# Performance work log

Measured on AMD Instinct MI355X. Metric: run time of the kernel, lower is better.

Reference implementation:

```python
import jax, jax.numpy as jnp
import numpy as np

N_NODES = 100000
N_EDGES = 1600000
IN_CH = 128
HID = 128
N_REL = 8


def setup_inputs() -> dict:
    key = jax.random.key(0)
    k_x, k_src, k_dst, k_et, k_w, k_root, k_b = jax.random.split(key, 7)
    x = jax.random.normal(k_x, (N_NODES, IN_CH), dtype=jnp.float32)
    src = jax.random.randint(k_src, (N_EDGES,), 0, N_NODES)
    dst = jax.random.randint(k_dst, (N_EDGES,), 0, N_NODES)
    edge_index = jnp.stack([src, dst], axis=0)  # [2, E]
    edge_type = jax.random.randint(k_et, (N_EDGES,), 0, N_REL)
    # RGCNConv parameters: per-relation weight, root (self-loop) weight, bias
    scale = 1.0 / np.sqrt(IN_CH)
    W = jax.random.normal(k_w, (N_REL, IN_CH, HID), dtype=jnp.float32) * scale
    root = jax.random.normal(k_root, (IN_CH, HID), dtype=jnp.float32) * scale
    bias = jnp.zeros((HID,), dtype=jnp.float32)
    return {"x": x, "edge_index": edge_index, "edge_type": edge_type,
            "W": W, "root": root, "bias": bias}


def reference(x, edge_index, edge_type, W, root, bias):
    # RGCNConv (mean aggregation per relation) + ReLU. Dropout is identity (eval mode).
    # Aggregate-then-transform: mathematically identical to PyG's
    # transform-then-aggregate since the relation transform is linear,
    # but far cheaper (R matmuls over N nodes instead of E edges).
    N = x.shape[0]
    n_rel = W.shape[0]
    src, dst = edge_index[0], edge_index[1]
    x_src = x[src]  # [E, C] gathered neighbor features
    out = x @ root + bias  # root / self-loop term
    for r in range(n_rel):
        mask = (edge_type == r)
        xm = jnp.where(mask[:, None], x_src, 0.0)  # zero out other relations
        agg = jax.ops.segment_sum(xm, dst, num_segments=N)  # [N, C]
        cnt = jax.ops.segment_sum(mask.astype(x.dtype), dst, num_segments=N)
        mean_agg = agg / jnp.maximum(cnt, 1.0)[:, None]
        out = out + mean_agg @ W[r]
    return jax.nn.relu(out)
```

## Files before the change

### kernel.cpp

```cpp
#include <hip/hip_runtime.h>

#define NREL 8
#define CH   128
#define YW   1152
#define YWD  (YW / 2)
#define NCB2 18
#define BTN  (YW * CH)

#define SCAN_ITEMS   16
#define SCAN_THREADS 256
#define SCAN_CHUNK   (SCAN_ITEMS * SCAN_THREADS)
#define SCAN_SHIFT   12

typedef short  short8v __attribute__((ext_vector_type(8)));
typedef float  f32x4   __attribute__((ext_vector_type(4)));

__device__ __forceinline__ unsigned short f2bf(float f) {
    union { float f; unsigned u; } v; v.f = f;
    return (unsigned short)((v.u + 0x7FFFu + ((v.u >> 16) & 1u)) >> 16);
}
__device__ __forceinline__ float lof(unsigned u) {
    union { unsigned u; float f; } v; v.u = u << 16; return v.f;
}
__device__ __forceinline__ float hif(unsigned u) {
    union { unsigned u; float f; } v; v.u = u & 0xFFFF0000u; return v.f;
}
__device__ __forceinline__ void gload_lds16(const void* g, void* l) {
    __builtin_amdgcn_global_load_lds(
        (const __attribute__((address_space(1))) unsigned int*)g,
        (__attribute__((address_space(3))) unsigned int*)l, 16, 0, 0);
}

__global__ __launch_bounds__(256) void hist_rank_bt2_kernel(
    const int* __restrict__ dst, const int* __restrict__ et,
    int* __restrict__ hist, int* __restrict__ rank, int E,
    const float* __restrict__ W, const float* __restrict__ root,
    unsigned short* __restrict__ Bt2)
{
    int e = blockIdx.x * blockDim.x + threadIdx.x;
    if (e < E) rank[e] = atomicAdd(&hist[dst[e] * NREL + et[e]], 1);
    if (e < BTN) {
        int rc = e >> 7, k = e & 127;
        int r = rc >> 7, c = rc & 127;
        float v = (r < NREL) ? W[(size_t)(r * CH + k) * CH + c]
                             : root[(size_t)k * CH + c];
        Bt2[e] = f2bf(v);
    }
}

__global__ __launch_bounds__(SCAN_THREADS) void scan1_kernel(
    const int* __restrict__ hist, int* __restrict__ pad_offs,
    int* __restrict__ partials, int S)
{
    __shared__ int lds[SCAN_THREADS];
    int t = threadIdx.x;
    int base = blockIdx.x * SCAN_CHUNK + t * SCAN_ITEMS;
    int v[SCAN_ITEMS];
    int s = 0;
#pragma unroll
    for (int j = 0; j < SCAN_ITEMS; j++) {
        int idx = base + j;
        int h = (idx < S) ? hist[idx] : 0;
        v[j] = s; s += h;
    }
    int run = s;
    lds[t] = run; __syncthreads();
    for (int off = 1; off < SCAN_THREADS; off <<= 1) {
        int y = (t >= off) ? lds[t - off] : 0;
        __syncthreads();
        run += y; lds[t] = run; __syncthreads();
    }
    int tb = run - s;
    if (t == SCAN_THREADS - 1) partials[blockIdx.x] = run;
#pragma unroll
    for (int j = 0; j < SCAN_ITEMS; j++) {
        int idx = base + j;
        if (idx < S) pad_offs[idx] = tb + v[j];
    }
}

__global__ __launch_bounds__(SCAN_THREADS) void scan2_kernel(
    int* __restrict__ partials, int NB, int* __restrict__ pad_offs,
    int S, int E)
{
    __shared__ int lds[SCAN_THREADS];
    int t = threadIdx.x;
    int s = (t < NB) ? partials[t] : 0;
    int run = s;
    lds[t] = run; __syncthreads();
    for (int off = 1; off < SCAN_THREADS; off <<= 1) {
        int y = (t >= off) ? lds[t - off] : 0;
        __syncthreads();
        run += y; lds[t] = run; __syncthreads();
    }
    if (t < NB) partials[t] = run - s;
    if (t == 0) pad_offs[S] = E;
}

__global__ __launch_bounds__(512, 6) void ygemm_fill_kernel(
    const float* __restrict__ x,
    const unsigned short* __restrict__ Bt2,
    unsigned short* __restrict__ y,
    int N,
    const int* __restrict__ src, const int* __restrict__ dst,
    const int* __restrict__ et, const int* __restrict__ rank,
    const int* __restrict__ pad_offs, const int* __restrict__ partials,
    int* __restrict__ perm, int E, int epb)
{
    __shared__ __align__(16) unsigned short As[128 * 128];
    __shared__ __align__(16) unsigned short Bs[64 * 128];

    int tid  = threadIdx.x;
    int lane = tid & 63;
    int wid  = tid >> 6;
    int wm   = wid >> 2;
    int wn   = wid & 3;
    int r15  = lane & 15;
    int kg   = lane >> 4;
    int n0   = blockIdx.x * 128;

    int eb   = blockIdx.x * epb;
    int elim = eb + epb; if (elim > E) elim = E;
    int p0 = -1, p1 = -1, p2 = -1, p3 = -1;
    int v0 = 0, v1 = 0, v2 = 0, v3 = 0;
    {
        int e0 = eb + tid;
        int e1 = e0 + 512, e2 = e1 + 512, e3 = e2 + 512;
        if (e0 < elim) { int t0 = et[e0]; v0 = (src[e0] << 3) | t0;
                         int sg = dst[e0] * NREL + t0;
                         p0 = pad_offs[sg] + partials[sg >> SCAN_SHIFT] + rank[e0]; }
        if (e1 < elim) { int t1 = et[e1]; v1 = (src[e1] << 3) | t1;
                         int sg = dst[e1] * NREL + t1;
                         p1 = pad_offs[sg] + partials[sg >> SCAN_SHIFT] + rank[e1]; }
        if (e2 < elim) { int t2 = et[e2]; v2 = (src[e2] << 3) | t2;
                         int sg = dst[e2] * NREL + t2;
                         p2 = pad_offs[sg] + partials[sg >> SCAN_SHIFT] + rank[e2]; }
        if (e3 < elim) { int t3 = et[e3]; v3 = (src[e3] << 3) | t3;
                         int sg = dst[e3] * NREL + t3;
                         p3 = pad_offs[sg] + partials[sg >> SCAN_SHIFT] + rank[e3]; }
    }

    {
        int row = tid >> 2;
        int kq  = tid & 3;
        int gn  = n0 + row; if (gn >= N) gn = N - 1;
        const float* xp = x + (size_t)gn * CH + kq * 32;
#pragma unroll
        for (int s8 = 0; s8 < 4; ++s8) {
            float4 f0 = *(const float4*)(xp + s8 * 8);
            float4 f1 = *(const float4*)(xp + s8 * 8 + 4);
            uint4 v;
            v.x = f2bf(f0.x) | ((unsigned)f2bf(f0.y) << 16);
            v.y = f2bf(f0.z) | ((unsigned)f2bf(f0.w) << 16);
            v.z = f2bf(f1.x) | ((unsigned)f2bf(f1.y) << 16);
            v.w = f2bf(f1.z) | ((unsigned)f2bf(f1.w) << 16);
            int slot = kq * 4 + s8;
            int phys = slot ^ (row & 15);
            *(uint4*)&As[row * 128 + phys * 8] = v;
        }
    }

    for (int cb = 0; cb < NCB2; ++cb) {
#pragma unroll
        for (int i = 0; i < 2; ++i) {
            int chunk = wid * 2 + i;
            int col   = chunk * 4 + (lane >> 4);
            int slot  = (lane & 15) ^ (col & 15);
            const char* srcp = (const char*)(Bt2 + (size_t)(cb * 64 + col) * CH + slot * 8);
            gload_lds16(srcp, &Bs[chunk * 512]);
        }
        __syncthreads();

        if      (cb == 1) { if (p0 >= 0) perm[p0] = v0; }
        else if (cb == 2) { if (p1 >= 0) perm[p1] = v1; }
        else if (cb == 3) { if (p2 >= 0) perm[p2] = v2; }
        else if (cb == 4) { if (p3 >= 0) perm[p3] = v3; }

        f32x4 acc[4];
#pragma unroll
        for (int i = 0; i < 4; i++) acc[i] = f32x4{0.f, 0.f, 0.f, 0.f};

#pragma unroll
        for (int ks = 0; ks < 4; ++ks) {
            short8v a[4], b;
#pragma unroll
            for (int mr = 0; mr < 4; ++mr) {
                int row  = wm * 64 + mr * 16 + r15;
                int phys = (ks * 4 + kg) ^ (row & 15);
                a[mr] = *(const short8v*)&As[row * 128 + phys * 8];
            }
            {
                int col  = wn * 16 + r15;
                int phys = (ks * 4 + kg) ^ (col & 15);
                b = *(const short8v*)&Bs[col * 128 + phys * 8];
            }
#pragma unroll
            for (int mr = 0; mr < 4; ++mr)
                acc[mr] = __builtin_amdgcn_mfma_f32_16x16x32_bf16(
                    a[mr], b, acc[mr], 0, 0, 0);
        }

#pragma unroll
        for (int mr = 0; mr < 4; ++mr) {
#pragma unroll
            for (int reg = 0; reg < 4; ++reg) {
                int gr = n0 + wm * 64 + mr * 16 + kg * 4 + reg;
                if (gr >= N) continue;
                int gc = cb * 64 + wn * 16 + r15;
                y[(size_t)gr * YW + gc] = f2bf(acc[mr][reg]);
            }
        }
        __syncthreads();
    }
}

__global__ __launch_bounds__(256) void gather_kernel(
    const unsigned short* __restrict__ y,
    const int* __restrict__ perm,
    const int* __restrict__ pad_offs,
    const int* __restrict__ partials,
    const int* __restrict__ hist,
    const float* __restrict__ bias,
    float* __restrict__ out, int N)
{
    int wid  = threadIdx.x >> 6;
    int lane = threadIdx.x & 63;
    int n    = blockIdx.x * 4 + wid;
    if (n >= N) return;

    int S  = N * NREL;
    int i0 = n * NREL;
    int i8 = i0 + NREL;
    int beg = pad_offs[i0] + partials[i0 >> SCAN_SHIFT];
    int end = pad_offs[i8] + ((i8 == S) ? 0 : partials[i8 >> SCAN_SHIFT]);

    int4 h0 = *(const int4*)(hist + (size_t)n * NREL);
    int4 h1 = *(const int4*)(hist + (size_t)n * NREL + 4);
    float iw0 = 1.0f / (float)max(h0.x, 1);
    float iw1 = 1.0f / (float)max(h0.y, 1);
    float iw2 = 1.0f / (float)max(h0.z, 1);
    float iw3 = 1.0f / (float)max(h0.w, 1);
    float iw4 = 1.0f / (float)max(h1.x, 1);
    float iw5 = 1.0f / (float)max(h1.y, 1);
    float iw6 = 1.0f / (float)max(h1.z, 1);
    float iw7 = 1.0f / (float)max(h1.w, 1);

    const unsigned* y32 = (const unsigned*)y;
    float a0 = 0.f, a1 = 0.f;

    for (int blk = beg; blk < end; blk += 64) {
        int m = end - blk; if (m > 64) m = 64;
        int   rv = 0;
        float wv = 0.f;
        if (lane < m) {
            int pv  = perm[blk + lane];
            int rel = pv & 7;
            rv = pv + (pv >> 3);
            float wa = (rel & 1) ? iw1 : iw0;
            float wb = (rel & 1) ? iw3 : iw2;
            float wc = (rel & 1) ? iw5 : iw4;
            float wd = (rel & 1) ? iw7 : iw6;
            float we_ = (rel & 2) ? wb : wa;
            float wf  = (rel & 2) ? wd : wc;
            wv = (rel & 4) ? wf : we_;
        }

        int j = 0;
#define EDGE_LOAD(K) \
            int   p##K = __shfl(rv, j + K);                     \
            float w##K = __shfl(wv, j + K);                     \
            unsigned u##K = y32[(size_t)p##K * 64 + lane];
#define EDGE_ACC(K) \
            a0 += w##K * lof(u##K); a1 += w##K * hif(u##K);

        for (; j + 16 <= m; j += 16) {
            EDGE_LOAD(0) EDGE_LOAD(1) EDGE_LOAD(2)  EDGE_LOAD(3)
            EDGE_LOAD(4) EDGE_LOAD(5) EDGE_LOAD(6)  EDGE_LOAD(7)
            EDGE_LOAD(8) EDGE_LOAD(9) EDGE_LOAD(10) EDGE_LOAD(11)
            EDGE_LOAD(12) EDGE_LOAD(13) EDGE_LOAD(14) EDGE_LOAD(15)
            EDGE_ACC(0)  EDGE_ACC(1)  EDGE_ACC(2)  EDGE_ACC(3)
            EDGE_ACC(4)  EDGE_ACC(5)  EDGE_ACC(6)  EDGE_ACC(7)
            EDGE_ACC(8)  EDGE_ACC(9)  EDGE_ACC(10) EDGE_ACC(11)
            EDGE_ACC(12) EDGE_ACC(13) EDGE_ACC(14) EDGE_ACC(15)
        }
        if (j + 8 <= m) {
            EDGE_LOAD(0) EDGE_LOAD(1) EDGE_LOAD(2) EDGE_LOAD(3)
            EDGE_LOAD(4) EDGE_LOAD(5) EDGE_LOAD(6) EDGE_LOAD(7)
            EDGE_ACC(0) EDGE_ACC(1) EDGE_ACC(2) EDGE_ACC(3)
            EDGE_ACC(4) EDGE_ACC(5) EDGE_ACC(6) EDGE_ACC(7)
            j += 8;
        }
        if (j + 4 <= m) {
            EDGE_LOAD(0) EDGE_LOAD(1) EDGE_LOAD(2) EDGE_LOAD(3)
            EDGE_ACC(0) EDGE_ACC(1) EDGE_ACC(2) EDGE_ACC(3)
            j += 4;
        }
        for (; j < m; ++j) {
            EDGE_LOAD(0)
            EDGE_ACC(0)
        }
#undef EDGE_LOAD
#undef EDGE_ACC
    }

    unsigned ur = y32[(size_t)n * YWD + (NREL * CH / 2) + lane];
    float o0 = a0 + lof(ur) + bias[lane * 2];
    float o1 = a1 + hif(ur) + bias[lane * 2 + 1];
    float2 ov;
    ov.x = fmaxf(o0, 0.f);
    ov.y = fmaxf(o1, 0.f);
    *(float2*)(out + (size_t)n * CH + lane * 2) = ov;
}

extern "C" void kernel_launch(void* const* d_in, const int* in_sizes, int n_in,
                              void* d_out, int out_size, void* d_ws, size_t ws_size,
                              hipStream_t stream)
{
    const float* x    = (const float*)d_in[0];
    const int*   ei   = (const int*)d_in[1];
    const int*   et   = (const int*)d_in[2];
    const float* W    = (const float*)d_in[3];
    const float* root = (const float*)d_in[4];
    const float* bias = (const float*)d_in[5];
    float*       out  = (float*)d_out;

    int N = in_sizes[0] / CH;
    int E = in_sizes[2];
    const int* src = ei;
    const int* dst = ei + E;

    int S  = N * NREL;
    int NB = (S + SCAN_CHUNK - 1) / SCAN_CHUNK;

    unsigned short* y   = (unsigned short*)d_ws;
    unsigned short* Bt2 = y + (size_t)N * YW;
    int* hist     = (int*)(Bt2 + (size_t)YW * CH);
    int* pad_offs = hist + S;
    int* partials = pad_offs + S + 1;
    int* perm     = partials + 256;
    int* rank     = perm + E;

    hipMemsetAsync(hist, 0, (size_t)S * sizeof(int), stream);

    int egrid = (E + 255) / 256;
    int G     = (N + 127) / 128;
    int epb   = ((E + G - 1) / G + 2047) & ~2047;

    hist_rank_bt2_kernel<<<egrid, 256, 0, stream>>>(dst, et, hist, rank, E,
                                                    W, root, Bt2);
    scan1_kernel<<<NB, SCAN_THREADS, 0, stream>>>(hist, pad_offs, partials, S);
    scan2_kernel<<<1, SCAN_THREADS, 0, stream>>>(partials, NB, pad_offs, S, E);
    ygemm_fill_kernel<<<G, 512, 0, stream>>>(x, Bt2, y, N,
                                             src, dst, et, rank, pad_offs,
                                             partials, perm, E, epb);
    gather_kernel<<<(N + 3) / 4, 256, 0, stream>>>(y, perm, pad_offs, partials,
                                                   hist, bias, out, N);
}
```

Baseline: 279.8 us.

## Enlarge ygemm M-tile to 256 rows with 4x2 MFMA per warp

Doubles the node tile per block from 128 to 256 rows and gives each wave a 64x32 output sub-tile (two B fragments), so each B column block loaded into shared memory is reused across more rows and fewer blocks re-fetch Bt2. The per-block edge scatter share doubles, handled with 8 per-thread perm entries written during the first 8 column blocks. Launch bounds drop to 4 blocks per CU because shared memory and registers per block grow. The trade-off is fewer blocks, about 391 for 100k nodes, which may underfill the GPU and reduce latency hiding.

```diff
diff --git a/kernel.cpp b/kernel.cpp
--- a/kernel.cpp
+++ b/kernel.cpp
@@ -6,6 +6,7 @@
 #define YWD  (YW / 2)
 #define NCB2 18
 #define BTN  (YW * CH)
+#define BM   256
 
 #define SCAN_ITEMS   16
 #define SCAN_THREADS 256
@@ -97,7 +98,7 @@
     if (t == 0) pad_offs[S] = E;
 }
 
-__global__ __launch_bounds__(512, 6) void ygemm_fill_kernel(
+__global__ __launch_bounds__(512, 4) void ygemm_fill_kernel(
     const float* __restrict__ x,
     const unsigned short* __restrict__ Bt2,
     unsigned short* __restrict__ y,
@@ -107,46 +108,40 @@
     const int* __restrict__ pad_offs, const int* __restrict__ partials,
     int* __restrict__ perm, int E, int epb)
 {
-    __shared__ __align__(16) unsigned short As[128 * 128];
+    __shared__ __align__(16) unsigned short As[BM * 128];
     __shared__ __align__(16) unsigned short Bs[64 * 128];
 
     int tid  = threadIdx.x;
     int lane = tid & 63;
     int wid  = tid >> 6;
-    int wm   = wid >> 2;
-    int wn   = wid & 3;
+    int wm   = wid >> 1;
+    int wn   = wid & 1;
     int r15  = lane & 15;
     int kg   = lane >> 4;
-    int n0   = blockIdx.x * 128;
+    int n0   = blockIdx.x * BM;
 
     int eb   = blockIdx.x * epb;
     int elim = eb + epb; if (elim > E) elim = E;
-    int p0 = -1, p1 = -1, p2 = -1, p3 = -1;
-    int v0 = 0, v1 = 0, v2 = 0, v3 = 0;
+    int pp[8], vv[8];
+#pragma unroll
+    for (int i = 0; i < 8; ++i) {
+        int e = eb + tid + i * 512;
+        pp[i] = -1; vv[i] = 0;
+        if (e < elim) {
+            int t0 = et[e];
+            vv[i] = (src[e] << 3) | t0;
+            int sg = dst[e] * NREL + t0;
+            pp[i] = pad_offs[sg] + partials[sg >> SCAN_SHIFT] + rank[e];
+        }
+    }
+
     {
-        int e0 = eb + tid;
-        int e1 = e0 + 512, e2 = e1 + 512, e3 = e2 + 512;
-        if (e0 < elim) { int t0 = et[e0]; v0 = (src[e0] << 3) | t0;
-                         int sg = dst[e0] * NREL + t0;
-                         p0 = pad_offs[sg] + partials[sg >> SCAN_SHIFT] + rank[e0]; }
-        if (e1 < elim) { int t1 = et[e1]; v1 = (src[e1] << 3) | t1;
-                         int sg = dst[e1] * NREL + t1;
-                         p1 = pad_offs[sg] + partials[sg >> SCAN_SHIFT] + rank[e1]; }
-        if (e2 < elim) { int t2 = et[e2]; v2 = (src[e2] << 3) | t2;
-                         int sg = dst[e2] * NREL + t2;
-                         p2 = pad_offs[sg] + partials[sg >> SCAN_SHIFT] + rank[e2]; }
-        if (e3 < elim) { int t3 = et[e3]; v3 = (src[e3] << 3) | t3;
-                         int sg = dst[e3] * NREL + t3;
-                         p3 = pad_offs[sg] + partials[sg >> SCAN_SHIFT] + rank[e3]; }
-    }
-
-    {
-        int row = tid >> 2;
-        int kq  = tid & 3;
-        int gn  = n0 + row; if (gn >= N) gn = N - 1;
-        const float* xp = x + (size_t)gn * CH + kq * 32;
-#pragma unroll
-        for (int s8 = 0; s8 < 4; ++s8) {
+        int row  = tid >> 1;
+        int half = tid & 1;
+        int gn   = n0 + row; if (gn >= N) gn = N - 1;
+        const float* xp = x + (size_t)gn * CH + half * 64;
+#pragma unroll
+        for (int s8 = 0; s8 < 8; ++s8) {
             float4 f0 = *(const float4*)(xp + s8 * 8);
             float4 f1 = *(const float4*)(xp + s8 * 8 + 4);
             uint4 v;
@@ -154,7 +149,7 @@
             v.y = f2bf(f0.z) | ((unsigned)f2bf(f0.w) << 16);
             v.z = f2bf(f1.x) | ((unsigned)f2bf(f1.y) << 16);
             v.w = f2bf(f1.z) | ((unsigned)f2bf(f1.w) << 16);
-            int slot = kq * 4 + s8;
+            int slot = half * 8 + s8;
             int phys = slot ^ (row & 15);
             *(uint4*)&As[row * 128 + phys * 8] = v;
         }
@@ -171,43 +166,52 @@
         }
         __syncthreads();
 
-        if      (cb == 1) { if (p0 >= 0) perm[p0] = v0; }
-        else if (cb == 2) { if (p1 >= 0) perm[p1] = v1; }
-        else if (cb == 3) { if (p2 >= 0) perm[p2] = v2; }
-        else if (cb == 4) { if (p3 >= 0) perm[p3] = v3; }
-
-        f32x4 acc[4];
-#pragma unroll
-        for (int i = 0; i < 4; i++) acc[i] = f32x4{0.f, 0.f, 0.f, 0.f};
+        if (cb >= 1 && cb <= 8) {
+            int i = cb - 1;
+            if (pp[i] >= 0) perm[pp[i]] = vv[i];
+        }
+
+        f32x4 acc[4][2];
+#pragma unroll
+        for (int i = 0; i < 4; i++)
+#pragma unroll
+            for (int j = 0; j < 2; j++)
+                acc[i][j] = f32x4{0.f, 0.f, 0.f, 0.f};
 
 #pragma unroll
         for (int ks = 0; ks < 4; ++ks) {
-            short8v a[4], b;
+            short8v a[4], b[2];
 #pragma unroll
             for (int mr = 0; mr < 4; ++mr) {
                 int row  = wm * 64 + mr * 16 + r15;
                 int phys = (ks * 4 + kg) ^ (row & 15);
                 a[mr] = *(const short8v*)&As[row * 128 + phys * 8];
             }
-            {
-                int col  = wn * 16 + r15;
+#pragma unroll
+            for (int nc = 0; nc < 2; ++nc) {
+                int col  = wn * 32 + nc * 16 + r15;
                 int phys = (ks * 4 + kg) ^ (col & 15);
-                b = *(const short8v*)&Bs[col * 128 + phys * 8];
+                b[nc] = *(const short8v*)&Bs[col * 128 + phys * 8];
             }
 #pragma unroll
             for (int mr = 0; mr < 4; ++mr)
-                acc[mr] = __builtin_amdgcn_mfma_f32_16x16x32_bf16(
-                    a[mr], b, acc[mr], 0, 0, 0);
+#pragma unroll
+                for (int nc = 0; nc < 2; ++nc)
+                    acc[mr][nc] = __builtin_amdgcn_mfma_f32_16x16x32_bf16(
+                        a[mr], b[nc], acc[mr][nc], 0, 0, 0);
         }
 
 #pragma unroll
         for (int mr = 0; mr < 4; ++mr) {
 #pragma unroll
-            for (int reg = 0; reg < 4; ++reg) {
-                int gr = n0 + wm * 64 + mr * 16 + kg * 4 + reg;
-                if (gr >= N) continue;
-                int gc = cb * 64 + wn * 16 + r15;
-                y[(size_t)gr * YW + gc] = f2bf(acc[mr][reg]);
+            for (int nc = 0; nc < 2; ++nc) {
+                int gc = cb * 64 + wn * 32 + nc * 16 + r15;
+#pragma unroll
+                for (int reg = 0; reg < 4; ++reg) {
+                    int gr = n0 + wm * 64 + mr * 16 + kg * 4 + reg;
+                    if (gr >= N) continue;
+                    y[(size_t)gr * YW + gc] = f2bf(acc[mr][nc][reg]);
+                }
             }
         }
         __syncthreads();
@@ -343,8 +347,8 @@
     hipMemsetAsync(hist, 0, (size_t)S * sizeof(int), stream);
 
     int egrid = (E + 255) / 256;
-    int G     = (N + 127) / 128;
-    int epb   = ((E + G - 1) / G + 2047) & ~2047;
+    int G     = (N + BM - 1) / BM;
+    int epb   = ((E + G - 1) / G + 4095) & ~4095;
 
     hist_rank_bt2_kernel<<<egrid, 256, 0, stream>>>(dst, et, hist, rank, E,
                                                     W, root, Bt2);
```

New measurement: 265.5 us, median of 5. 5.1% less time.
